# Optimization experiments

Measured on AMD Instinct MI355X. Metric: run time of the kernel, lower is better.

## Reference

```python
import jax, jax.numpy as jnp
import numpy as np

K = 64            # number of keypoints
PATCH = 16        # patch size
NUM_CLASSES = 1000
K_HARRIS = 0.04


def _conv3x3(x, w):
    # x: [N, Cin, H, W], w: [Cout, Cin, 3, 3], stride 1, padding 1 (torch conv2d = cross-correlation)
    return jax.lax.conv_general_dilated(x, w, (1, 1), 'SAME',
                                        dimension_numbers=('NCHW', 'OIHW', 'NCHW'))


def _harris_coords(x, k, patch_size):
    B, C, H, W = x.shape
    g = jnp.mean(x, axis=1, keepdims=True) if C != 1 else x  # grayscale [B,1,H,W]
    dxk = jnp.array([[-1., 0., 1.], [-1., 0., 1.], [-1., 0., 1.]], x.dtype).reshape(1, 1, 3, 3)
    dyk = jnp.array([[-1., -1., -1.], [0., 0., 0.], [1., 1., 1.]], x.dtype).reshape(1, 1, 3, 3)
    gauss = (jnp.array([[1., 2., 1.], [2., 4., 2.], [1., 2., 1.]], x.dtype) / 16.0).reshape(1, 1, 3, 3)
    dx = _conv3x3(g, dxk)
    dy = _conv3x3(g, dyk)
    Sxx = _conv3x3(dx * dx, gauss)
    Syy = _conv3x3(dy * dy, gauss)
    Sxy = _conv3x3(dx * dy, gauss)
    R = Sxx * Syy - Sxy ** 2 - K_HARRIS * (Sxx + Syy) ** 2  # [B,1,H,W]
    m = patch_size
    mask = jnp.zeros((H, W), x.dtype).at[m:H - m, m:W - m].set(1.0)
    R_flat = (R[:, 0] * mask).reshape(B, -1)
    _, idx = jax.lax.top_k(R_flat, k)                        # [B,k]
    coords = jnp.stack([idx // W, idx % W], axis=-1).astype(jnp.float32)  # (row, col)
    coords = (coords / jnp.array([H, W], jnp.float32) - 0.5) * 2.0
    return jnp.clip(coords, -1.0, 1.0)                       # [B,k,2]


def _grid_sample_bilinear(img, grid):
    # img: [N,C,H,W]; grid: [N,Hg,Wg,2] with (x, y) in [-1,1]; align_corners=True, zeros padding
    N, C, H, W = img.shape
    Hg, Wg = grid.shape[1], grid.shape[2]
    gx = (grid[..., 0] + 1.0) * 0.5 * (W - 1)
    gy = (grid[..., 1] + 1.0) * 0.5 * (H - 1)
    x0 = jnp.floor(gx); y0 = jnp.floor(gy)
    x1 = x0 + 1.0;      y1 = y0 + 1.0
    wx1 = gx - x0; wx0 = 1.0 - wx1
    wy1 = gy - y0; wy0 = 1.0 - wy1

    img_flat = img.reshape(N, C, H * W)

    def gather(xi, yi):
        valid = ((xi >= 0) & (xi < W) & (yi >= 0) & (yi < H)).astype(img.dtype)
        xc = jnp.clip(xi, 0, W - 1).astype(jnp.int32)
        yc = jnp.clip(yi, 0, H - 1).astype(jnp.int32)
        flat = (yc * W + xc).reshape(N, 1, Hg * Wg)
        vals = jnp.take_along_axis(img_flat, flat, axis=2).reshape(N, C, Hg, Wg)
        return vals * valid[:, None]

    out = (gather(x0, y0) * (wx0 * wy0)[:, None]
           + gather(x1, y0) * (wx1 * wy0)[:, None]
           + gather(x0, y1) * (wx0 * wy1)[:, None]
           + gather(x1, y1) * (wx1 * wy1)[:, None])
    return out


def _extract_patches(images, keypoints, patch_size):
    B, C, H, W = images.shape
    k = keypoints.shape[1]
    coords01 = (keypoints + 1.0) / 2.0                       # [B,k,2] (y,x) in [0,1]
    r = patch_size / H
    pg = jnp.linspace(-r, r, patch_size)
    yy, xx = jnp.meshgrid(pg, pg, indexing='ij')
    base = jnp.stack([xx, yy], axis=-1)[None, None]          # [1,1,P,P,2] (x_off, y_off)
    grid = base + coords01[:, :, None, None, :]              # faithful to original broadcast
    grid = grid * 2.0 - 1.0
    grid = grid.reshape(B * k, patch_size, patch_size, 2)
    x_exp = jnp.repeat(images, k, axis=0)                    # repeat_interleave on batch
    patches = _grid_sample_bilinear(x_exp, grid)             # [B*k,C,P,P]
    return patches.reshape(B, k, C, patch_size, patch_size)


def _classify(patches, conv_w, conv_b, fc1_w, fc1_b, fc2_w, fc2_b):
    B, k, C, H, W = patches.shape
    p = patches.reshape(B * k, C, H, W)
    h = _conv3x3(p, conv_w) + conv_b[None, :, None, None]
    h = jax.nn.relu(h)
    h = h.reshape(B * k, -1)                                 # [B*k, 8*P*P]
    h = jax.nn.relu(h @ fc1_w.T + fc1_b)                     # [B*k, 64]
    h = h.reshape(B, k * 64)
    return h @ fc2_w.T + fc2_b                               # [B, num_classes]


def setup_inputs() -> dict:
    key = jax.random.key(0)
    ks = jax.random.split(key, 7)
    B, C, H, W = 32, 3, 224, 224
    return {
        'x': jax.random.normal(ks[0], (B, C, H, W), dtype=jnp.float32),
        'conv_w': jax.random.normal(ks[1], (8, C, 3, 3), dtype=jnp.float32) * 0.1,
        'conv_b': jax.random.normal(ks[2], (8,), dtype=jnp.float32) * 0.05,
        'fc1_w': jax.random.normal(ks[3], (64, 8 * PATCH * PATCH), dtype=jnp.float32) * 0.02,
        'fc1_b': jax.random.normal(ks[4], (64,), dtype=jnp.float32) * 0.05,
        'fc2_w': jax.random.normal(ks[5], (NUM_CLASSES, 64 * K), dtype=jnp.float32) * 0.02,
        'fc2_b': jax.random.normal(ks[6], (NUM_CLASSES,), dtype=jnp.float32) * 0.05,
    }


def reference(x, conv_w, conv_b, fc1_w, fc1_b, fc2_w, fc2_b):
    coords = _harris_coords(x, K, PATCH)                     # [B,K,2]
    patches = _extract_patches(x, coords, PATCH)             # [B,K,C,P,P]
    return _classify(patches, conv_w, conv_b, fc1_w, fc1_b, fc2_w, fc2_b)
```

## Files before the change

kernel.cpp:

```cpp
#include <hip/hip_runtime.h>
#include <cstdint>
#include <math.h>

#define HW 224
#define NPIX (HW*HW)
#define BATCH 32
#define KP 64
#define PS 16
#define NCLS 1000
#define TKW 112
#define TK_CHUNK (NPIX / TKW)
#define TK_ITERS (TK_CHUNK / 64)
#define FC1_KS 16

__global__ __launch_bounds__(256) void k_harris(const float* __restrict__ x,
                                                float* __restrict__ R) {
    const int bx = blockIdx.x, by = blockIdx.y, b = blockIdx.z;
    __shared__ float G[20][21];
    __shared__ float DX[18][19];
    __shared__ float DY[18][19];
    const int tid = threadIdx.x;
    const float* xb = x + (size_t)b * 3 * NPIX;

    for (int l = tid; l < 400; l += 256) {
        int p = l / 20, q = l % 20;
        int gy = by * 16 + p - 2, gx = bx * 16 + q - 2;
        float v = 0.f;
        if (gy >= 0 && gy < HW && gx >= 0 && gx < HW) {
            int o = gy * HW + gx;
            v = (xb[o] + xb[NPIX + o] + xb[2 * NPIX + o]) / 3.0f;
        }
        G[p][q] = v;
    }
    __syncthreads();

    for (int l = tid; l < 324; l += 256) {
        int a = l / 18, c = l % 18;
        int gy = by * 16 + a - 1, gx = bx * 16 + c - 1;
        float dxv = 0.f, dyv = 0.f;
        if (gy >= 0 && gy < HW && gx >= 0 && gx < HW) {
            dxv = (G[a][c + 2] - G[a][c]) + (G[a + 1][c + 2] - G[a + 1][c]) +
                  (G[a + 2][c + 2] - G[a + 2][c]);
            dyv = (G[a + 2][c] + G[a + 2][c + 1] + G[a + 2][c + 2]) -
                  (G[a][c] + G[a][c + 1] + G[a][c + 2]);
        }
        DX[a][c] = dxv;
        DY[a][c] = dyv;
    }
    __syncthreads();

    const int ty = tid / 16, tx = tid % 16;
    const int gy = by * 16 + ty, gx = bx * 16 + tx;
    float outv = 0.f;
    if (gy >= PS && gy < HW - PS && gx >= PS && gx < HW - PS) {
        const float gw[3][3] = {{1.f/16.f, 2.f/16.f, 1.f/16.f},
                                {2.f/16.f, 4.f/16.f, 2.f/16.f},
                                {1.f/16.f, 2.f/16.f, 1.f/16.f}};
        float sxx = 0.f, syy = 0.f, sxy = 0.f;
        #pragma unroll
        for (int u = 0; u < 3; u++)
            #pragma unroll
            for (int v = 0; v < 3; v++) {
                float dv = DX[ty + u][tx + v];
                float ev = DY[ty + u][tx + v];
                float w = gw[u][v];
                sxx += w * dv * dv;
                syy += w * ev * ev;
                sxy += w * dv * ev;
            }
        float tr = sxx + syy;
        outv = sxx * syy - sxy * sxy - 0.04f * tr * tr;
    }
    R[(size_t)b * NPIX + gy * HW + gx] = outv;
}

__device__ __forceinline__ uint64_t tk_pack(float v, int idx) {
    uint32_t u = __float_as_uint(v);
    u = (u & 0x80000000u) ? ~u : (u | 0x80000000u);
    return ((uint64_t)u << 32) | (uint32_t)(~idx);
}

__device__ __forceinline__ uint64_t tk_sort_asc(uint64_t k, int lane) {
    #pragma unroll
    for (int size = 2; size <= 64; size <<= 1) {
        #pragma unroll
        for (int stride = size >> 1; stride >= 1; stride >>= 1) {
            uint64_t o = __shfl_xor(k, stride, 64);
            bool up = ((lane & size) == 0);
            bool keepmax = (((lane & stride) != 0) == up);
            k = keepmax ? (k > o ? k : o) : (k < o ? k : o);
        }
    }
    return k;
}

__device__ __forceinline__ uint64_t tk_clean_desc(uint64_t k, int lane) {
    #pragma unroll
    for (int stride = 32; stride >= 1; stride >>= 1) {
        uint64_t o = __shfl_xor(k, stride, 64);
        bool keepmax = ((lane & stride) == 0);
        k = keepmax ? (k > o ? k : o) : (k < o ? k : o);
    }
    return k;
}

__global__ __launch_bounds__(256) void k_topk_part(const float* __restrict__ R,
                                                   uint64_t* __restrict__ cand) {
    const int img = blockIdx.y;
    const int wave = blockIdx.x * 4 + (threadIdx.x >> 6);
    const int lane = threadIdx.x & 63;
    const float* base = R + (size_t)img * NPIX + wave * TK_CHUNK;
    const int idx_base = wave * TK_CHUNK + lane;

    uint64_t T = 0;
    #pragma unroll 1
    for (int it = 0; it < TK_ITERS; it++) {
        float v = base[it * 64 + lane];
        uint64_t ck = tk_pack(v, idx_base + it * 64);
        uint64_t thr = __shfl(T, 63, 64);
        if (__ballot(ck > thr)) {
            uint64_t s = tk_sort_asc(ck, lane);
            uint64_t m = (T > s) ? T : s;
            T = tk_clean_desc(m, lane);
        }
    }
    cand[((size_t)img * TKW + wave) * 64 + lane] = T;
}

__global__ __launch_bounds__(1024) void k_topk_merge(const uint64_t* __restrict__ cand,
                                                     int* __restrict__ kp) {
    const int img = blockIdx.x;
    const int w = threadIdx.x >> 6, lane = threadIdx.x & 63;
    const uint64_t* cb = cand + (size_t)img * TKW * 64;
    __shared__ uint64_t S[16 * 64];

    uint64_t T = cb[(w * 7) * 64 + lane];
    #pragma unroll
    for (int r = 1; r < 7; r++) {
        uint64_t C = cb[(w * 7 + r) * 64 + (63 - lane)];
        uint64_t m = (T > C) ? T : C;
        T = tk_clean_desc(m, lane);
    }
    S[w * 64 + lane] = T;
    __syncthreads();
    if (w == 0) {
        uint64_t T2 = S[lane];
        #pragma unroll
        for (int r = 1; r < 16; r++) {
            uint64_t C = S[r * 64 + (63 - lane)];
            uint64_t m = (T2 > C) ? T2 : C;
            T2 = tk_clean_desc(m, lane);
        }
        kp[img * KP + lane] = (int)(~(uint32_t)T2);
    }
}

__device__ __forceinline__ float gat4(const float* img, float xf, float yf) {
    bool valid = (xf >= 0.f) && (xf < 224.f) && (yf >= 0.f) && (yf < 224.f);
    if (!valid) return 0.f;
    int xi = (int)fminf(fmaxf(xf, 0.f), 223.f);
    int yi = (int)fminf(fmaxf(yf, 0.f), 223.f);
    return img[yi * HW + xi];
}

__global__ __launch_bounds__(256) void k_patch_conv(
    const float* __restrict__ x, const int* __restrict__ kp,
    const float* __restrict__ conv_w, const float* __restrict__ conv_b,
    float* __restrict__ h) {
    const int s = blockIdx.x;
    const int b = blockIdx.y;
    const int tid = threadIdx.x;

    __shared__ float P[3][16][16];
    __shared__ float CW[216];
    __shared__ float CB[8];
    for (int l = tid; l < 216; l += 256) CW[l] = conv_w[l];
    if (tid < 8) CB[tid] = conv_b[tid];

    const int idx = kp[b * KP + s];
    const int row = idx / HW, col = idx % HW;
    float cy = ((float)row / 224.0f - 0.5f) * 2.0f;
    float cx = ((float)col / 224.0f - 0.5f) * 2.0f;
    cy = fminf(fmaxf(cy, -1.0f), 1.0f);
    cx = fminf(fmaxf(cx, -1.0f), 1.0f);
    const float y01 = (cy + 1.0f) * 0.5f;
    const float x01 = (cx + 1.0f) * 0.5f;
    const float rr = 16.0f / 224.0f;
    const float step = (2.0f * rr) / 15.0f;
    const float* xb = x + (size_t)b * 3 * NPIX;

    for (int e = tid; e < 768; e += 256) {
        int c = e >> 8, rem = e & 255, i = rem >> 4, j = rem & 15;
        float pj = (j == 15) ? rr : (-rr + (float)j * step);
        float pi = (i == 15) ? rr : (-rr + (float)i * step);
        float gxn = (pj + y01) * 2.0f - 1.0f;
        float gyn = (pi + x01) * 2.0f - 1.0f;
        float gx = (gxn + 1.0f) * 0.5f * 223.0f;
        float gy = (gyn + 1.0f) * 0.5f * 223.0f;
        float x0 = floorf(gx), y0 = floorf(gy);
        float x1 = x0 + 1.0f, y1 = y0 + 1.0f;
        float wx1 = gx - x0, wy1 = gy - y0;
        float wx0 = 1.0f - wx1, wy0 = 1.0f - wy1;
        const float* img = xb + (size_t)c * NPIX;
        float acc = gat4(img, x0, y0) * (wx0 * wy0)
                  + gat4(img, x1, y0) * (wx1 * wy0)
                  + gat4(img, x0, y1) * (wx0 * wy1)
                  + gat4(img, x1, y1) * (wx1 * wy1);
        P[c][i][j] = acc;
    }
    __syncthreads();

    const int i = tid >> 4, j = tid & 15;
    const size_t mbase = ((size_t)(b * KP + s)) * 2048;
    #pragma unroll
    for (int co = 0; co < 8; co++) {
        float acc = CB[co];
        #pragma unroll
        for (int ci = 0; ci < 3; ci++)
            #pragma unroll
            for (int di = 0; di < 3; di++)
                #pragma unroll
                for (int dj = 0; dj < 3; dj++) {
                    int yy = i + di - 1, xx = j + dj - 1;
                    if (yy >= 0 && yy < 16 && xx >= 0 && xx < 16)
                        acc += P[ci][yy][xx] * CW[co * 27 + ci * 9 + di * 3 + dj];
                }
        h[mbase + co * 256 + tid] = fmaxf(acc, 0.0f);
    }
}

__global__ __launch_bounds__(256) void k_fc1(
    const float* __restrict__ h, const float* __restrict__ fc1_w,
    float* __restrict__ partial) {
    const int mt = blockIdx.x;
    const int ks = blockIdx.y;
    const int tid = threadIdx.x;
    const int M0 = mt * 64;
    const int og = tid >> 4, mg = tid & 15;
    __shared__ float A[64 * 68];
    __shared__ float W[64 * 68];
    float acc[4][4];
    #pragma unroll
    for (int i = 0; i < 4; i++)
        #pragma unroll
        for (int j = 0; j < 4; j++) acc[i][j] = 0.f;

    #pragma unroll 1
    for (int ch = 0; ch < 2; ch++) {
        const int k0 = ks * 128 + ch * 64;
        __syncthreads();
        #pragma unroll
        for (int p = 0; p < 4; p++) {
            int row = p * 16 + (tid >> 4);
            int c0 = (tid & 15) * 4;
            float4 av = *(const float4*)&h[(size_t)(M0 + row) * 2048 + k0 + c0];
            A[(c0 + 0) * 68 + row] = av.x;
            A[(c0 + 1) * 68 + row] = av.y;
            A[(c0 + 2) * 68 + row] = av.z;
            A[(c0 + 3) * 68 + row] = av.w;
            float4 wv = *(const float4*)&fc1_w[(size_t)row * 2048 + k0 + c0];
            W[(c0 + 0) * 68 + row] = wv.x;
            W[(c0 + 1) * 68 + row] = wv.y;
            W[(c0 + 2) * 68 + row] = wv.z;
            W[(c0 + 3) * 68 + row] = wv.w;
        }
        __syncthreads();
        #pragma unroll 4
        for (int k = 0; k < 64; k++) {
            float4 a = *(float4*)&A[k * 68 + mg * 4];
            float4 w = *(float4*)&W[k * 68 + og * 4];
            acc[0][0] += a.x * w.x; acc[0][1] += a.x * w.y;
            acc[0][2] += a.x * w.z; acc[0][3] += a.x * w.w;
            acc[1][0] += a.y * w.x; acc[1][1] += a.y * w.y;
            acc[1][2] += a.y * w.z; acc[1][3] += a.y * w.w;
            acc[2][0] += a.z * w.x; acc[2][1] += a.z * w.y;
            acc[2][2] += a.z * w.z; acc[2][3] += a.z * w.w;
            acc[3][0] += a.w * w.x; acc[3][1] += a.w * w.y;
            acc[3][2] += a.w * w.z; acc[3][3] += a.w * w.w;
        }
    }
    float* pb = partial + ((size_t)ks * 2048 + M0) * 64;
    #pragma unroll
    for (int mi = 0; mi < 4; mi++) {
        float4 v = make_float4(acc[mi][0], acc[mi][1], acc[mi][2], acc[mi][3]);
        *(float4*)&pb[(mg * 4 + mi) * 64 + og * 4] = v;
    }
}

__global__ __launch_bounds__(256) void k_fc1_post(
    const float* __restrict__ partial, const float* __restrict__ fc1_b,
    float* __restrict__ featT) {
    const int id = blockIdx.x * 256 + threadIdx.x;
    const int o = id & 63, m = id >> 6;
    float s = 0.f;
    #pragma unroll
    for (int ks = 0; ks < FC1_KS; ks++) s += partial[(size_t)ks * 131072 + id];
    s = fmaxf(s + fc1_b[o], 0.f);
    featT[(size_t)((m & 63) * 64 + o) * 32 + (m >> 6)] = s;
}

__global__ __launch_bounds__(256) void k_bias(const float* __restrict__ fc2_b,
                                              float* __restrict__ out) {
    int id = blockIdx.x * 256 + threadIdx.x;
    if (id < BATCH * NCLS) out[id] = fc2_b[id % NCLS];
}

__global__ __launch_bounds__(256) void k_fc2(
    const float* __restrict__ featT, const float* __restrict__ fc2_w,
    float* __restrict__ out) {
    const int c0 = blockIdx.x * 8;
    const int kbase = blockIdx.y * 512;
    const int tid = threadIdx.x;
    const int b = tid & 31, kg = tid >> 5;
    __shared__ float F[128 * 36];
    __shared__ float Wc[8 * 128];
    __shared__ float Red[8 * 8 * 32];

    float acc[8];
    #pragma unroll
    for (int cl = 0; cl < 8; cl++) acc[cl] = 0.f;

    #pragma unroll 1
    for (int ch = 0; ch < 4; ch++) {
        const int k0 = kbase + ch * 128;
        __syncthreads();
        #pragma unroll
        for (int r = 0; r < 4; r++) {
            int l = tid + r * 256;
            int f = l >> 3, b4 = (l & 7) << 2;
            *(float4*)&F[f * 36 + b4] =
                *(const float4*)&featT[(size_t)(k0 + f) * 32 + b4];
        }
        {
            int cl = tid >> 5, koff = (tid & 31) << 2;
            *(float4*)&Wc[cl * 128 + koff] =
                *(const float4*)&fc2_w[(size_t)(c0 + cl) * 4096 + k0 + koff];
        }
        __syncthreads();
        #pragma unroll
        for (int cl = 0; cl < 8; cl++) {
            #pragma unroll
            for (int i = 0; i < 16; i += 4) {
                float4 wv = *(float4*)&Wc[cl * 128 + kg * 16 + i];
                int f = kg * 16 + i;
                acc[cl] += wv.x * F[f * 36 + b] + wv.y * F[(f + 1) * 36 + b] +
                           wv.z * F[(f + 2) * 36 + b] + wv.w * F[(f + 3) * 36 + b];
            }
        }
    }
    __syncthreads();
    #pragma unroll
    for (int cl = 0; cl < 8; cl++) Red[(kg * 8 + cl) * 32 + b] = acc[cl];
    __syncthreads();
    const int cl2 = tid >> 5, b2 = tid & 31;
    float s = 0.f;
    #pragma unroll
    for (int g = 0; g < 8; g++) s += Red[(g * 8 + cl2) * 32 + b2];
    atomicAdd(&out[b2 * NCLS + c0 + cl2], s);
}

extern "C" void kernel_launch(void* const* d_in, const int* in_sizes, int n_in,
                              void* d_out, int out_size, void* d_ws, size_t ws_size,
                              hipStream_t stream) {
    const float* x      = (const float*)d_in[0];
    const float* conv_w = (const float*)d_in[1];
    const float* conv_b = (const float*)d_in[2];
    const float* fc1_w  = (const float*)d_in[3];
    const float* fc1_b  = (const float*)d_in[4];
    const float* fc2_w  = (const float*)d_in[5];
    const float* fc2_b  = (const float*)d_in[6];
    float* out = (float*)d_out;

    char* base = (char*)d_ws;
    const size_t region0 = (size_t)FC1_KS * 2048 * 64 * 4;
    float*    R       = (float*)base;
    uint64_t* cand    = (uint64_t*)(base + (size_t)BATCH * NPIX * 4);
    float*    partial = (float*)base;
    float*    h       = (float*)(base + region0);
    float*    featT   = h + (size_t)2048 * 2048;
    int*      kp      = (int*)(featT + (size_t)4096 * 32);

    k_harris<<<dim3(14, 14, 32), 256, 0, stream>>>(x, R);
    k_topk_part<<<dim3(28, 32), 256, 0, stream>>>(R, cand);
    k_topk_merge<<<32, 1024, 0, stream>>>(cand, kp);
    k_patch_conv<<<dim3(KP, BATCH), 256, 0, stream>>>(x, kp, conv_w, conv_b, h);
    k_fc1<<<dim3(32, FC1_KS), 256, 0, stream>>>(h, fc1_w, partial);
    k_fc1_post<<<512, 256, 0, stream>>>(partial, fc1_b, featT);
    k_bias<<<(BATCH * NCLS + 255) / 256, 256, 0, stream>>>(fc2_b, out);
    k_fc2<<<dim3(125, 8), 256, 0, stream>>>(featT, fc2_w, out);
}
```

Before: 186.5 us.

## Fuse Harris response with partial top-k and fold bias init into fc1_post

Combines the Harris response and per-chunk top-k into one kernel. Each block computes 8 full rows of R in shared memory and runs the wave-level bitonic top-k directly on them, so the full R map is never written to or read back from global memory. The fc2 bias initialisation is folded into k_fc1_post, removing one launch. The fc2 K-split is doubled to 16 slices, which adds parallelism but also doubles the atomicAdds. Shared memory per block grows to about 33 KB, which may reduce occupancy.

```diff
diff --git a/kernel.cpp b/kernel.cpp
--- a/kernel.cpp
+++ b/kernel.cpp
@@ -9,70 +9,7 @@
 #define PS 16
 #define NCLS 1000
 #define TKW 112
-#define TK_CHUNK (NPIX / TKW)
-#define TK_ITERS (TK_CHUNK / 64)
 #define FC1_KS 16
-
-__global__ __launch_bounds__(256) void k_harris(const float* __restrict__ x,
-                                                float* __restrict__ R) {
-    const int bx = blockIdx.x, by = blockIdx.y, b = blockIdx.z;
-    __shared__ float G[20][21];
-    __shared__ float DX[18][19];
-    __shared__ float DY[18][19];
-    const int tid = threadIdx.x;
-    const float* xb = x + (size_t)b * 3 * NPIX;
-
-    for (int l = tid; l < 400; l += 256) {
-        int p = l / 20, q = l % 20;
-        int gy = by * 16 + p - 2, gx = bx * 16 + q - 2;
-        float v = 0.f;
-        if (gy >= 0 && gy < HW && gx >= 0 && gx < HW) {
-            int o = gy * HW + gx;
-            v = (xb[o] + xb[NPIX + o] + xb[2 * NPIX + o]) / 3.0f;
-        }
-        G[p][q] = v;
-    }
-    __syncthreads();
-
-    for (int l = tid; l < 324; l += 256) {
-        int a = l / 18, c = l % 18;
-        int gy = by * 16 + a - 1, gx = bx * 16 + c - 1;
-        float dxv = 0.f, dyv = 0.f;
-        if (gy >= 0 && gy < HW && gx >= 0 && gx < HW) {
-            dxv = (G[a][c + 2] - G[a][c]) + (G[a + 1][c + 2] - G[a + 1][c]) +
-                  (G[a + 2][c + 2] - G[a + 2][c]);
-            dyv = (G[a + 2][c] + G[a + 2][c + 1] + G[a + 2][c + 2]) -
-                  (G[a][c] + G[a][c + 1] + G[a][c + 2]);
-        }
-        DX[a][c] = dxv;
-        DY[a][c] = dyv;
-    }
-    __syncthreads();
-
-    const int ty = tid / 16, tx = tid % 16;
-    const int gy = by * 16 + ty, gx = bx * 16 + tx;
-    float outv = 0.f;
-    if (gy >= PS && gy < HW - PS && gx >= PS && gx < HW - PS) {
-        const float gw[3][3] = {{1.f/16.f, 2.f/16.f, 1.f/16.f},
-                                {2.f/16.f, 4.f/16.f, 2.f/16.f},
-                                {1.f/16.f, 2.f/16.f, 1.f/16.f}};
-        float sxx = 0.f, syy = 0.f, sxy = 0.f;
-        #pragma unroll
-        for (int u = 0; u < 3; u++)
-            #pragma unroll
-            for (int v = 0; v < 3; v++) {
-                float dv = DX[ty + u][tx + v];
-                float ev = DY[ty + u][tx + v];
-                float w = gw[u][v];
-                sxx += w * dv * dv;
-                syy += w * ev * ev;
-                sxy += w * dv * ev;
-            }
-        float tr = sxx + syy;
-        outv = sxx * syy - sxy * sxy - 0.04f * tr * tr;
-    }
-    R[(size_t)b * NPIX + gy * HW + gx] = outv;
-}
 
 __device__ __forceinline__ uint64_t tk_pack(float v, int idx) {
     uint32_t u = __float_as_uint(v);
@@ -104,19 +41,82 @@
     return k;
 }
 
-__global__ __launch_bounds__(256) void k_topk_part(const float* __restrict__ R,
-                                                   uint64_t* __restrict__ cand) {
-    const int img = blockIdx.y;
-    const int wave = blockIdx.x * 4 + (threadIdx.x >> 6);
-    const int lane = threadIdx.x & 63;
-    const float* base = R + (size_t)img * NPIX + wave * TK_CHUNK;
-    const int idx_base = wave * TK_CHUNK + lane;
-
+__global__ __launch_bounds__(256) void k_harris_topk(const float* __restrict__ x,
+                                                     uint64_t* __restrict__ cand) {
+    const int r = blockIdx.x, b = blockIdx.y;
+    const int tid = threadIdx.x;
+    const int row0 = r * 8;
+    __shared__ float G[12][228];
+    __shared__ float DXs[10][228];
+    __shared__ float DYs[10][228];
+    __shared__ float RB[1792];
+    const float* xb = x + (size_t)b * 3 * NPIX;
+
+    for (int l = tid; l < 12 * 224; l += 256) {
+        int gr = l / 224, gc = l % 224;
+        int gy = row0 - 2 + gr;
+        float v = 0.f;
+        if (gy >= 0 && gy < HW) {
+            int o = gy * HW + gc;
+            v = (xb[o] + xb[NPIX + o] + xb[2 * NPIX + o]) / 3.0f;
+        }
+        G[gr][gc + 1] = v;
+    }
+    if (tid < 12) { G[tid][0] = 0.f; G[tid][225] = 0.f; }
+    if (tid < 10) { DXs[tid][0] = 0.f; DXs[tid][225] = 0.f;
+                    DYs[tid][0] = 0.f; DYs[tid][225] = 0.f; }
+    __syncthreads();
+
+    for (int l = tid; l < 10 * 224; l += 256) {
+        int dr = l / 224, dc = l % 224;
+        int ay = row0 - 1 + dr;
+        float dxv = 0.f, dyv = 0.f;
+        if (ay >= 0 && ay < HW) {
+            dxv = (G[dr][dc + 2] - G[dr][dc]) + (G[dr + 1][dc + 2] - G[dr + 1][dc]) +
+                  (G[dr + 2][dc + 2] - G[dr + 2][dc]);
+            dyv = (G[dr + 2][dc] + G[dr + 2][dc + 1] + G[dr + 2][dc + 2]) -
+                  (G[dr][dc] + G[dr][dc + 1] + G[dr][dc + 2]);
+        }
+        DXs[dr][dc + 1] = dxv;
+        DYs[dr][dc + 1] = dyv;
+    }
+    __syncthreads();
+
+    for (int l = tid; l < 1792; l += 256) {
+        int rr = l / 224, c = l % 224;
+        int gy = row0 + rr;
+        float outv = 0.f;
+        if (gy >= PS && gy < HW - PS && c >= PS && c < HW - PS) {
+            const float gw[3][3] = {{1.f/16.f, 2.f/16.f, 1.f/16.f},
+                                    {2.f/16.f, 4.f/16.f, 2.f/16.f},
+                                    {1.f/16.f, 2.f/16.f, 1.f/16.f}};
+            float sxx = 0.f, syy = 0.f, sxy = 0.f;
+            #pragma unroll
+            for (int u = 0; u < 3; u++)
+                #pragma unroll
+                for (int v = 0; v < 3; v++) {
+                    float dv = DXs[rr + u][c + v];
+                    float ev = DYs[rr + u][c + v];
+                    float w = gw[u][v];
+                    sxx += w * dv * dv;
+                    syy += w * ev * ev;
+                    sxy += w * dv * ev;
+                }
+            float tr = sxx + syy;
+            outv = sxx * syy - sxy * sxy - 0.04f * tr * tr;
+        }
+        RB[l] = outv;
+    }
+    __syncthreads();
+
+    const int w = tid >> 6, lane = tid & 63;
+    const int chunk = w * 448;
+    const int gbase = row0 * 224 + chunk;
     uint64_t T = 0;
     #pragma unroll 1
-    for (int it = 0; it < TK_ITERS; it++) {
-        float v = base[it * 64 + lane];
-        uint64_t ck = tk_pack(v, idx_base + it * 64);
+    for (int it = 0; it < 7; it++) {
+        float v = RB[chunk + it * 64 + lane];
+        uint64_t ck = tk_pack(v, gbase + it * 64 + lane);
         uint64_t thr = __shfl(T, 63, 64);
         if (__ballot(ck > thr)) {
             uint64_t s = tk_sort_asc(ck, lane);
@@ -124,7 +124,7 @@
             T = tk_clean_desc(m, lane);
         }
     }
-    cand[((size_t)img * TKW + wave) * 64 + lane] = T;
+    cand[((size_t)b * TKW + r * 4 + w) * 64 + lane] = T;
 }
 
 __global__ __launch_bounds__(1024) void k_topk_merge(const uint64_t* __restrict__ cand,
@@ -289,7 +289,8 @@
 
 __global__ __launch_bounds__(256) void k_fc1_post(
     const float* __restrict__ partial, const float* __restrict__ fc1_b,
-    float* __restrict__ featT) {
+    const float* __restrict__ fc2_b, float* __restrict__ featT,
+    float* __restrict__ out) {
     const int id = blockIdx.x * 256 + threadIdx.x;
     const int o = id & 63, m = id >> 6;
     float s = 0.f;
@@ -297,11 +298,6 @@
     for (int ks = 0; ks < FC1_KS; ks++) s += partial[(size_t)ks * 131072 + id];
     s = fmaxf(s + fc1_b[o], 0.f);
     featT[(size_t)((m & 63) * 64 + o) * 32 + (m >> 6)] = s;
-}
-
-__global__ __launch_bounds__(256) void k_bias(const float* __restrict__ fc2_b,
-                                              float* __restrict__ out) {
-    int id = blockIdx.x * 256 + threadIdx.x;
     if (id < BATCH * NCLS) out[id] = fc2_b[id % NCLS];
 }
 
@@ -309,7 +305,7 @@
     const float* __restrict__ featT, const float* __restrict__ fc2_w,
     float* __restrict__ out) {
     const int c0 = blockIdx.x * 8;
-    const int kbase = blockIdx.y * 512;
+    const int kbase = blockIdx.y * 256;
     const int tid = threadIdx.x;
     const int b = tid & 31, kg = tid >> 5;
     __shared__ float F[128 * 36];
@@ -321,7 +317,7 @@
     for (int cl = 0; cl < 8; cl++) acc[cl] = 0.f;
 
     #pragma unroll 1
-    for (int ch = 0; ch < 4; ch++) {
+    for (int ch = 0; ch < 2; ch++) {
         const int k0 = kbase + ch * 128;
         __syncthreads();
         #pragma unroll
@@ -373,19 +369,16 @@
 
     char* base = (char*)d_ws;
     const size_t region0 = (size_t)FC1_KS * 2048 * 64 * 4;
-    float*    R       = (float*)base;
-    uint64_t* cand    = (uint64_t*)(base + (size_t)BATCH * NPIX * 4);
+    uint64_t* cand    = (uint64_t*)base;
     float*    partial = (float*)base;
     float*    h       = (float*)(base + region0);
     float*    featT   = h + (size_t)2048 * 2048;
     int*      kp      = (int*)(featT + (size_t)4096 * 32);
 
-    k_harris<<<dim3(14, 14, 32), 256, 0, stream>>>(x, R);
-    k_topk_part<<<dim3(28, 32), 256, 0, stream>>>(R, cand);
+    k_harris_topk<<<dim3(28, 32), 256, 0, stream>>>(x, cand);
     k_topk_merge<<<32, 1024, 0, stream>>>(cand, kp);
     k_patch_conv<<<dim3(KP, BATCH), 256, 0, stream>>>(x, kp, conv_w, conv_b, h);
     k_fc1<<<dim3(32, FC1_KS), 256, 0, stream>>>(h, fc1_w, partial);
-    k_fc1_post<<<512, 256, 0, stream>>>(partial, fc1_b, featT);
-    k_bias<<<(BATCH * NCLS + 255) / 256, 256, 0, stream>>>(fc2_b, out);
-    k_fc2<<<dim3(125, 8), 256, 0, stream>>>(featT, fc2_w, out);
-}
+    k_fc1_post<<<512, 256, 0, stream>>>(partial, fc1_b, fc2_b, featT, out);
+    k_fc2<<<dim3(125, 16), 256, 0, stream>>>(featT, fc2_w, out);
+}
```

After: 186.0 us. Within noise of the previous version (-0.3%).
